# Kernel tuning notes

Measured on AMD Instinct MI355X. Metric: run time of the kernel, lower is better.

## Reference

```python
import jax, jax.numpy as jnp
import numpy as np

V, L, H, D, S, B = 32000, 6, 16, 1024, 512, 4
DK = D // H
DF = 4 * D
EPS = 1e-5


def setup_inputs() -> dict:
    key = jax.random.key(0)
    ks = jax.random.split(key, 24)
    std = 0.02
    def w(k, shape):
        return jax.random.normal(k, shape, dtype=jnp.float32) * std
    inp = {
        'x': jax.random.randint(ks[0], (B, S), 0, V),
        'tok_emb': w(ks[1], (V, D)),
        # per-layer params stacked on leading L axis; Linear stored as [in,out]
        'wq': w(ks[2], (L, D, D)), 'bq': jnp.zeros((L, D)),
        'wk': w(ks[3], (L, D, D)), 'bk': jnp.zeros((L, D)),
        'wv': w(ks[4], (L, D, D)), 'bv': jnp.zeros((L, D)),
        'wo': w(ks[5], (L, D, D)), 'bo': jnp.zeros((L, D)),
        'ln1_g': jnp.ones((L, D)), 'ln1_b': jnp.zeros((L, D)),
        'w1': w(ks[6], (L, D, DF)), 'b1': jnp.zeros((L, DF)),
        'w2': w(ks[7], (L, DF, D)), 'b2': jnp.zeros((L, D)),
        'ln2_g': jnp.ones((L, D)), 'ln2_b': jnp.zeros((L, D)),
        'lnf_g': jnp.ones((D,)), 'lnf_b': jnp.zeros((D,)),
        'lm_w': w(ks[8], (D, V)),
    }
    return inp


def _layernorm(x, g, b):
    mu = jnp.mean(x, axis=-1, keepdims=True)
    var = jnp.mean(jnp.square(x - mu), axis=-1, keepdims=True)
    return (x - mu) * jax.lax.rsqrt(var + EPS) * g + b


def _sinusoidal_pe(seq_len, d_model):
    pos = jnp.arange(seq_len, dtype=jnp.float32)[:, None]
    div = jnp.exp(jnp.arange(0, d_model, 2, dtype=jnp.float32) * (-np.log(10000.0) / d_model))
    pe = jnp.zeros((seq_len, d_model), dtype=jnp.float32)
    pe = pe.at[:, 0::2].set(jnp.sin(pos * div))
    pe = pe.at[:, 1::2].set(jnp.cos(pos * div))
    return pe  # [S, D]


def _gpt_forward(x, tok_emb, wq, bq, wk, bk, wv, bv, wo, bo,
                 ln1_g, ln1_b, w1, b1, w2, b2, ln2_g, ln2_b,
                 lnf_g, lnf_b, lm_w):
    b, s = x.shape
    h = tok_emb[x] + _sinusoidal_pe(s, D)  # [B,S,D]
    causal = jnp.tril(jnp.ones((s, s), dtype=bool))  # True = keep
    scale = 1.0 / np.sqrt(DK)

    def block(h, p):
        (wq, bq, wk, bk, wv, bv, wo, bo,
         ln1_g, ln1_b, w1, b1, w2, b2, ln2_g, ln2_b) = p
        hn = _layernorm(h, ln1_g, ln1_b)
        q = (hn @ wq + bq).reshape(b, s, H, DK)
        k = (hn @ wk + bk).reshape(b, s, H, DK)
        v = (hn @ wv + bv).reshape(b, s, H, DK)
        scores = jnp.einsum('bqhd,bkhd->bhqk', q, k) * scale
        scores = jnp.where(causal, scores, -1e9)
        attn = jax.nn.softmax(scores, axis=-1)
        ctx = jnp.einsum('bhqk,bkhd->bqhd', attn, v).reshape(b, s, D)
        h = h + (ctx @ wo + bo)
        hn2 = _layernorm(h, ln2_g, ln2_b)
        ff = jax.nn.gelu(hn2 @ w1 + b1, approximate=False) @ w2 + b2
        return h + ff, None

    params = (wq, bq, wk, bk, wv, bv, wo, bo,
              ln1_g, ln1_b, w1, b1, w2, b2, ln2_g, ln2_b)
    h, _ = jax.lax.scan(block, h, params)
    h = _layernorm(h, lnf_g, lnf_b)
    return h @ lm_w  # [B,S,V] logits


def reference(x, tok_emb, wq, bq, wk, bk, wv, bv, wo, bo,
              ln1_g, ln1_b, w1, b1, w2, b2, ln2_g, ln2_b,
              lnf_g, lnf_b, lm_w):
    return _gpt_forward(x, tok_emb, wq, bq, wk, bk, wv, bv, wo, bo,
                        ln1_g, ln1_b, w1, b1, w2, b2, ln2_g, ln2_b,
                        lnf_g, lnf_b, lm_w)
```

## Files before the change

kernel.cpp:

```cpp
#include <hip/hip_runtime.h>
#include <hip/hip_bf16.h>
#include <math.h>

#define V_SIZE 32000
#define L_NUM 6
#define H_NUM 16
#define D_MODEL 1024
#define S_LEN 512
#define B_SZ 4
#define DF_DIM 4096
#define ROWS (B_SZ * S_LEN)
#define QKV_N (3 * D_MODEL)
#define KVBLK 64
#define NJOB 12

typedef unsigned short u16;
typedef __attribute__((ext_vector_type(8))) short short8v;
typedef __attribute__((ext_vector_type(4))) float f32x4;

__device__ __forceinline__ float b2f(u16 b) {
  union { float f; unsigned u; } c; c.u = ((unsigned)b) << 16; return c.f;
}
__device__ __forceinline__ u16 f2b(float f) {
  __hip_bfloat16 h = __float2bfloat16(f);
  union { __hip_bfloat16 h; u16 u; } c; c.h = h; return c.u;
}
__device__ __forceinline__ void g2l16(const void* g, void* l) {
  __builtin_amdgcn_global_load_lds(
      (const __attribute__((address_space(1))) void*)g,
      (__attribute__((address_space(3))) void*)l, 16, 0, 0);
}

__global__ __launch_bounds__(256) void embed_kernel(
    const int* __restrict__ x, const float* __restrict__ tok_emb,
    float* __restrict__ h) {
  int row = blockIdx.x;
  int s = row % S_LEN;
  int tok = x[row];
  const float* te = tok_emb + (size_t)tok * D_MODEL;
  float* hr = h + (size_t)row * D_MODEL;
  float pos = (float)s;
  const float c = 9.210340371976184f / (float)D_MODEL;
#pragma unroll
  for (int i = 0; i < D_MODEL / 256; ++i) {
    int d = threadIdx.x + i * 256;
    float freq = expf(-(float)(d & ~1) * c);
    float ang = pos * freq;
    float pe = (d & 1) ? cosf(ang) : sinf(ang);
    hr[d] = te[d] + pe;
  }
}

__global__ __launch_bounds__(256) void layernorm_kernel(
    const float* __restrict__ in, const float* __restrict__ g,
    const float* __restrict__ b, u16* __restrict__ out) {
  const int row = blockIdx.x * 4 + (threadIdx.x >> 6);
  const int lane = threadIdx.x & 63;
  const float4* xr = (const float4*)(in + (size_t)row * D_MODEL);
  float4 v[4];
  float s1 = 0.f, s2 = 0.f;
#pragma unroll
  for (int i = 0; i < 4; ++i) {
    float4 t = xr[lane + i * 64];
    v[i] = t;
    s1 += t.x + t.y + t.z + t.w;
    s2 += t.x * t.x + t.y * t.y + t.z * t.z + t.w * t.w;
  }
#pragma unroll
  for (int off = 32; off; off >>= 1) {
    s1 += __shfl_xor(s1, off, 64);
    s2 += __shfl_xor(s2, off, 64);
  }
  const float mu = s1 * (1.0f / D_MODEL);
  const float var = s2 * (1.0f / D_MODEL) - mu * mu;
  const float rstd = rsqrtf(var + 1e-5f);
  u16* orow = out + (size_t)row * D_MODEL;
#pragma unroll
  for (int i = 0; i < 4; ++i) {
    const int d = (lane + i * 64) * 4;
    const float4 gv = *(const float4*)&g[d];
    const float4 bv = *(const float4*)&b[d];
    u16 o0 = f2b((v[i].x - mu) * rstd * gv.x + bv.x);
    u16 o1 = f2b((v[i].y - mu) * rstd * gv.y + bv.y);
    u16 o2 = f2b((v[i].z - mu) * rstd * gv.z + bv.z);
    u16 o3 = f2b((v[i].w - mu) * rstd * gv.w + bv.w);
    uint2 pk;
    pk.x = (unsigned)o0 | ((unsigned)o1 << 16);
    pk.y = (unsigned)o2 | ((unsigned)o3 << 16);
    *(uint2*)&orow[d] = pk;
  }
}

__global__ __launch_bounds__(256) void transpose_cvt(
    const float* __restrict__ W, u16* __restrict__ Wt, int K, int N,
    long out_stride) {
  __shared__ float t[64][33];
  const float* Wl = W + (size_t)blockIdx.z * K * N;
  u16* Wtl = Wt + (size_t)blockIdx.z * out_stride;
  const int n0 = blockIdx.x * 32, k0 = blockIdx.y * 64;
  const int tx = threadIdx.x & 31, ty = threadIdx.x >> 5;
#pragma unroll
  for (int i = 0; i < 64; i += 8)
    t[ty + i][tx] = Wl[(size_t)(k0 + ty + i) * N + n0 + tx];
  __syncthreads();
#pragma unroll
  for (int j = 0; j < 32; j += 8) {
    const int n = ty + j;
    u16 lo = f2b(t[2 * tx][n]);
    u16 hi = f2b(t[2 * tx + 1][n]);
    *(unsigned*)&Wtl[(size_t)(n0 + n) * K + k0 + 2 * tx] =
        (unsigned)lo | ((unsigned)hi << 16);
  }
}

__global__ __launch_bounds__(256) void pack_qkv_bias(
    const float* __restrict__ bq, const float* __restrict__ bk,
    const float* __restrict__ bv, float* __restrict__ out) {
  int i = blockIdx.x * 256 + threadIdx.x;
  int l = i / QKV_N, j = i % QKV_N;
  float v = (j < D_MODEL) ? bq[l * D_MODEL + j]
          : (j < 2 * D_MODEL) ? bk[l * D_MODEL + j - D_MODEL]
          : bv[l * D_MODEL + j - 2 * D_MODEL];
  out[i] = v;
}

template <int TM, int OUT_MODE, bool GELU_ACT, int SPLITK>
__global__ __launch_bounds__(256) void gemm_bf16(
    const u16* __restrict__ A, const u16* __restrict__ Bt,
    const float* __restrict__ bias, float* __restrict__ Cf,
    u16* __restrict__ Cb, int M, int N, int K) {
  constexpr int MF = TM / 32;
  constexpr int AINSTS = TM / 32;
  __shared__ __align__(16) u16 As[2][TM * 64];
  __shared__ __align__(16) u16 Bs[2][128 * 64];
  const int tid = threadIdx.x;
  const int wid = tid >> 6;
  const int lane = tid & 63;
  const int wr = wid >> 1, wc = wid & 1;
  const int nwg = gridDim.x;
  const int id = blockIdx.x;
  const int q = nwg >> 3, r = nwg & 7;
  const int xcd = id & 7, i0 = id >> 3;
  const int swz = (xcd < r ? xcd * (q + 1) : r * (q + 1) + (xcd - r) * q) + i0;
  const int kh = (SPLITK > 1) ? (swz & (SPLITK - 1)) : 0;
  const int rest = (SPLITK > 1) ? (swz >> 1) : swz;
  const int gm = M / TM;
  const int bm = rest % gm, bn = rest / gm;
  const int Ksub = K / SPLITK;
  const int rowi = lane >> 3;
  const int gsw = ((lane & 7) ^ rowi) * 8;
  const u16* Ag = A + (size_t)(bm * TM + wid * (TM / 4) + rowi) * K + kh * Ksub + gsw;
  const u16* Bg = Bt + (size_t)(bn * 128 + wid * 32 + rowi) * K + kh * Ksub + gsw;
  auto stage = [&](int buf, int k0) {
#pragma unroll
    for (int i = 0; i < AINSTS; ++i)
      g2l16(Ag + k0 + (size_t)(8 * i) * K, As[buf] + wid * (TM / 4) * 64 + i * 512);
#pragma unroll
    for (int i = 0; i < 4; ++i)
      g2l16(Bg + k0 + (size_t)(8 * i) * K, Bs[buf] + wid * 2048 + i * 512);
  };
  f32x4 acc[MF][4] = {};
  const int fr = lane & 15;
  const int hi = lane >> 4;
  stage(0, 0);
  __syncthreads();
  for (int k0 = 0; k0 < Ksub; k0 += 64) {
    const int cur = (k0 >> 6) & 1;
    if (k0 + 64 < Ksub) stage(cur ^ 1, k0 + 64);
    short8v a[MF][2], b[4][2];
#pragma unroll
    for (int m = 0; m < MF; ++m)
#pragma unroll
      for (int kk = 0; kk < 2; ++kk) {
        const int g = (kk * 4 + hi) ^ (fr & 7);
        a[m][kk] = *(const short8v*)&As[cur][(wr * (TM / 2) + m * 16 + fr) * 64 + g * 8];
      }
#pragma unroll
    for (int n = 0; n < 4; ++n)
#pragma unroll
      for (int kk = 0; kk < 2; ++kk) {
        const int g = (kk * 4 + hi) ^ (fr & 7);
        b[n][kk] = *(const short8v*)&Bs[cur][(wc * 64 + n * 16 + fr) * 64 + g * 8];
      }
    __builtin_amdgcn_s_setprio(1);
#pragma unroll
    for (int kk = 0; kk < 2; ++kk)
#pragma unroll
      for (int m = 0; m < MF; ++m)
#pragma unroll
        for (int n = 0; n < 4; ++n)
          acc[m][n] = __builtin_amdgcn_mfma_f32_16x16x32_bf16(a[m][kk], b[n][kk], acc[m][n], 0, 0, 0);
    __builtin_amdgcn_s_setprio(0);
    __syncthreads();
  }
  const int row0 = bm * TM + wr * (TM / 2) + hi * 4;
  const int col0 = bn * 128 + wc * 64 + fr;
#pragma unroll
  for (int m = 0; m < MF; ++m) {
#pragma unroll
    for (int n = 0; n < 4; ++n) {
      const int col = col0 + n * 16;
      float bv = (OUT_MODE == 2) ? 0.f : bias[col];
      if (SPLITK > 1 && kh != 0) bv = 0.f;
#pragma unroll
      for (int r2 = 0; r2 < 4; ++r2) {
        const int row = row0 + m * 16 + r2;
        float v = acc[m][n][r2] + bv;
        if (GELU_ACT) v = 0.5f * v * (1.0f + erff(v * 0.70710678118f));
        size_t idx = (size_t)row * N + col;
        if (OUT_MODE == 0) Cb[idx] = f2b(v);
        else if (OUT_MODE == 1) {
          if (SPLITK > 1) atomicAdd(&Cf[idx], v);
          else Cf[idx] += v;
        } else Cf[idx] = v;
      }
    }
  }
}

#define LDA_H(H)                                                            \
  _Pragma("unroll") for (int m = 0; m < 4; ++m)                             \
  _Pragma("unroll") for (int ks = 0; ks < 2; ++ks) {                        \
    const int row_ = wm * 128 + (H)*64 + m * 16 + fr;                       \
    const int g_ = (ks * 4 + hi) ^ (fr & 7);                                \
    a[m][ks] = *(const short8v*)&smem[cur * 16384 + row_ * 64 + g_ * 8];    \
  }
#define LDB_H(H)                                                            \
  _Pragma("unroll") for (int n = 0; n < 2; ++n)                             \
  _Pragma("unroll") for (int ks = 0; ks < 2; ++ks) {                        \
    const int row_ = wn * 64 + (H)*32 + n * 16 + fr;                        \
    const int g_ = (ks * 4 + hi) ^ (fr & 7);                                \
    b[n][ks] = *(const short8v*)&smem[32768 + cur * 16384 + row_ * 64 + g_ * 8]; \
  }
#define MFMA_CLUSTER(QA, QB)                                                \
  __builtin_amdgcn_s_barrier();                                             \
  asm volatile("s_waitcnt lgkmcnt(0)" ::: "memory");                        \
  __builtin_amdgcn_sched_barrier(0);                                        \
  __builtin_amdgcn_s_setprio(1);                                            \
  _Pragma("unroll") for (int ks = 0; ks < 2; ++ks)                          \
  _Pragma("unroll") for (int m = 0; m < 4; ++m)                             \
  _Pragma("unroll") for (int n = 0; n < 2; ++n)                             \
    acc[(QA)*4 + m][(QB)*2 + n] = __builtin_amdgcn_mfma_f32_16x16x32_bf16(  \
        a[m][ks], b[n][ks], acc[(QA)*4 + m][(QB)*2 + n], 0, 0, 0);          \
  __builtin_amdgcn_s_setprio(0);

__global__ __launch_bounds__(512, 2) void gemm256_lm(
    const u16* __restrict__ A, const u16* __restrict__ Bt,
    float* __restrict__ C, int M, int N, int K) {
  extern __shared__ __align__(16) u16 smem[];
  const int tid = threadIdx.x, wid = tid >> 6, lane = tid & 63;
  const int wm = wid >> 2, wn = wid & 3;
  const int fr = lane & 15, hi = lane >> 4;
  const int T = K / 64;
  const int nwg = gridDim.x, id = blockIdx.x;
  const int q = nwg >> 3, r = nwg & 7;
  const int xcd = id & 7, i0 = id >> 3;
  const int swz = (xcd < r ? xcd * (q + 1) : r * (q + 1) + (xcd - r) * q) + i0;
  const int gm = M / 256;
  const int bm = swz % gm, bn = swz / gm;
  const int rowA0 = bm * 256, rowB0 = bn * 256;
  const int rowoff = wid * 8 + (lane >> 3);
  const int gsw = ((lane & 7) ^ (lane >> 3)) * 8;
  auto stA = [&](int qq, int tt, int bb) {
    g2l16(A + (size_t)(rowA0 + qq * 64 + rowoff) * K + tt * 64 + gsw,
          smem + bb * 16384 + qq * 4096 + wid * 512);
  };
  auto stB = [&](int qq, int tt, int bb) {
    g2l16(Bt + (size_t)(rowB0 + qq * 64 + rowoff) * K + tt * 64 + gsw,
          smem + 32768 + bb * 16384 + qq * 4096 + wid * 512);
  };
  f32x4 acc[8][4] = {};
  stA(0, 0, 0); stA(2, 0, 0);
  stB(0, 0, 0); stB(1, 0, 0); stB(2, 0, 0); stB(3, 0, 0);
  stA(1, 0, 0); stA(3, 0, 0);
  if (T > 1) {
    stA(0, 1, 1); stA(2, 1, 1);
    asm volatile("s_waitcnt vmcnt(2)" ::: "memory");
  } else {
    asm volatile("s_waitcnt vmcnt(0)" ::: "memory");
  }
  __builtin_amdgcn_s_barrier();
  for (int t = 0; t < T; ++t) {
    const int cur = t & 1, nxt = cur ^ 1;
    short8v a[4][2], b[2][2];
    LDA_H(0); LDB_H(0);
    if (t + 1 < T) { stB(0, t + 1, nxt); stB(1, t + 1, nxt); }
    MFMA_CLUSTER(0, 0);
    __builtin_amdgcn_s_barrier();
    LDB_H(1);
    if (t + 1 < T) { stB(2, t + 1, nxt); stB(3, t + 1, nxt); }
    MFMA_CLUSTER(0, 1);
    __builtin_amdgcn_s_barrier();
    LDA_H(1);
    if (t + 1 < T) { stA(1, t + 1, nxt); stA(3, t + 1, nxt); }
    MFMA_CLUSTER(1, 1);
    __builtin_amdgcn_s_barrier();
    LDB_H(0);
    if (t + 2 < T) { stA(0, t + 2, cur); stA(2, t + 2, cur); }
    MFMA_CLUSTER(1, 0);
    if (t + 1 < T) {
      if (t + 2 < T) asm volatile("s_waitcnt vmcnt(2)" ::: "memory");
      else           asm volatile("s_waitcnt vmcnt(0)" ::: "memory");
      __builtin_amdgcn_s_barrier();
    }
  }
  float* lf = (float*)smem;
#pragma unroll
  for (int c = 0; c < 2; ++c) {
    __syncthreads();
    if (wm == c) {
#pragma unroll
      for (int m = 0; m < 8; ++m)
#pragma unroll
        for (int n = 0; n < 4; ++n)
#pragma unroll
          for (int rr = 0; rr < 4; ++rr)
            lf[(m * 16 + hi * 4 + rr) * 256 + wn * 64 + n * 16 + fr] =
                acc[m][n][rr];
    }
    __syncthreads();
#pragma unroll
    for (int i = 0; i < 16; ++i) {
      const int f = i * 2048 + tid * 4;
      const int rw = f >> 8, cl = f & 255;
      f32x4 v = *(const f32x4*)&lf[f];
      __builtin_nontemporal_store(
          v, (f32x4*)&C[(size_t)(rowA0 + c * 128 + rw) * N + rowB0 + cl]);
    }
  }
}

__global__ __launch_bounds__(256) void attn_part(
    const u16* __restrict__ qkv, float* __restrict__ Op,
    float* __restrict__ Ml) {
  __shared__ __align__(16) u16 smem[3 * 64 * 72];
  u16 (*Qs)[72] = (u16(*)[72])smem;
  u16 (*Ks)[72] = (u16(*)[72])(smem + 4608);
  u16 (*Vs)[72] = (u16(*)[72])(smem + 9216);
  const int job = blockIdx.x, bh = blockIdx.y;
  constexpr int qt_of[NJOB] = {0, 1, 2, 3, 4, 4, 5, 5, 6, 6, 7, 7};
  constexpr int ch_of[NJOB] = {0, 0, 0, 0, 0, 1, 0, 1, 0, 1, 0, 1};
  const int qt = qt_of[job], ch = ch_of[job];
  const int b = bh >> 4, h = bh & 15;
  const int tid = threadIdx.x, wid = tid >> 6, lane = tid & 63;
  const int fr = lane & 15, ko = (lane >> 4) * 8;
  u16 (*Ps)[72] = (u16(*)[72])(smem + wid * 1152);
  const size_t rb = (size_t)b * S_LEN;
  const int q0 = qt * 64;
  const int hq = h * 64;
  const int t_lo = ch * 4;
  const int t_hi = (qt + 1 < t_lo + 4) ? qt + 1 : t_lo + 4;
#pragma unroll
  for (int i = 0; i < 2; ++i) {
    int e = tid + i * 256, r = e >> 3, c = (e & 7) * 8;
    *(short8v*)&Qs[r][c] = *(const short8v*)&qkv[(rb + q0 + r) * QKV_N + hq + c];
  }
  __syncthreads();
  short8v qf[2];
#pragma unroll
  for (int ks = 0; ks < 2; ++ks)
    qf[ks] = *(const short8v*)&Qs[wid * 16 + fr][ks * 32 + ko];
  f32x4 acc_o[4] = {};
  float mrow[4], lrow[4];
#pragma unroll
  for (int r = 0; r < 4; ++r) { mrow[r] = -1e30f; lrow[r] = 0.f; }
  short8v kreg[2], vreg[2];
  auto loadregs = [&](int t) {
    const int k0 = t * KVBLK;
#pragma unroll
    for (int i = 0; i < 2; ++i) {
      const int e = tid + i * 256, rr = e >> 3, cc = (e & 7) * 8;
      kreg[i] = *(const short8v*)&qkv[(rb + k0 + rr) * QKV_N + D_MODEL + hq + cc];
      vreg[i] = *(const short8v*)&qkv[(rb + k0 + rr) * QKV_N + 2 * D_MODEL + hq + cc];
    }
  };
  loadregs(t_lo);
  for (int t = t_lo; t < t_hi; ++t) {
    __syncthreads();
#pragma unroll
    for (int i = 0; i < 2; ++i) {
      const int e = tid + i * 256, rr = e >> 3, cc = (e & 7) * 8;
      *(short8v*)&Ks[rr][cc] = kreg[i];
#pragma unroll
      for (int j = 0; j < 8; ++j) Vs[cc + j][rr] = (u16)vreg[i][j];
    }
    __syncthreads();
    if (t + 1 < t_hi) loadregs(t + 1);
    const int k0 = t * KVBLK;
    f32x4 s[4] = {};
    __builtin_amdgcn_s_setprio(1);
#pragma unroll
    for (int n = 0; n < 4; ++n)
#pragma unroll
      for (int ks = 0; ks < 2; ++ks) {
        short8v kf = *(const short8v*)&Ks[n * 16 + fr][ks * 32 + ko];
        s[n] = __builtin_amdgcn_mfma_f32_16x16x32_bf16(qf[ks], kf, s[n], 0, 0, 0);
      }
    __builtin_amdgcn_s_setprio(0);
    const int rbase = q0 + wid * 16 + (lane >> 4) * 4;
#pragma unroll
    for (int r = 0; r < 4; ++r) {
      const int row_g = rbase + r;
      float vmax = -1e30f;
#pragma unroll
      for (int n = 0; n < 4; ++n) {
        float v = s[n][r] * 0.125f;
        if (k0 + n * 16 + fr > row_g) v = -1e30f;
        s[n][r] = v;
        vmax = fmaxf(vmax, v);
      }
#pragma unroll
      for (int off = 1; off < 16; off <<= 1) vmax = fmaxf(vmax, __shfl_xor(vmax, off, 64));
      const float mnew = fmaxf(mrow[r], vmax);
      const float sc = expf(mrow[r] - mnew);
      mrow[r] = mnew;
      float ssum = 0.f;
#pragma unroll
      for (int n = 0; n < 4; ++n) {
        float p = expf(s[n][r] - mnew);
        s[n][r] = p;
        ssum += p;
      }
#pragma unroll
      for (int off = 1; off < 16; off <<= 1) ssum += __shfl_xor(ssum, off, 64);
      lrow[r] = lrow[r] * sc + ssum;
#pragma unroll
      for (int n = 0; n < 4; ++n) {
        acc_o[n][r] *= sc;
        Ps[(lane >> 4) * 4 + r][n * 16 + fr] = f2b(s[n][r]);
      }
    }
    __builtin_amdgcn_s_setprio(1);
#pragma unroll
    for (int ks = 0; ks < 2; ++ks) {
      short8v pf = *(const short8v*)&Ps[fr][ks * 32 + ko];
#pragma unroll
      for (int n = 0; n < 4; ++n) {
        short8v vf = *(const short8v*)&Vs[n * 16 + fr][ks * 32 + ko];
        acc_o[n] = __builtin_amdgcn_mfma_f32_16x16x32_bf16(pf, vf, acc_o[n], 0, 0, 0);
      }
    }
    __builtin_amdgcn_s_setprio(0);
  }
  const size_t jb = (size_t)(bh * NJOB + job);
#pragma unroll
  for (int r = 0; r < 4; ++r) {
    const int row_l = wid * 16 + (lane >> 4) * 4 + r;
    const size_t base = (jb * 64 + row_l) * 64;
#pragma unroll
    for (int n = 0; n < 4; ++n) Op[base + n * 16 + fr] = acc_o[n][r];
    if (fr == 0) {
      Ml[jb * 128 + row_l * 2] = mrow[r];
      Ml[jb * 128 + row_l * 2 + 1] = lrow[r];
    }
  }
}

__global__ __launch_bounds__(256) void attn_combine(
    const float* __restrict__ Op, const float* __restrict__ Ml,
    u16* __restrict__ ctx) {
  const int qt = blockIdx.x, bh = blockIdx.y;
  const int b = bh >> 4, h = bh & 15;
  constexpr int job0_of[8] = {0, 1, 2, 3, 4, 6, 8, 10};
  const int j0 = job0_of[qt];
  const bool two = qt >= 4;
  const size_t rb = (size_t)b * S_LEN;
  const int q0 = qt * 64, hq = h * 64;
  const size_t jb1 = (size_t)(bh * NJOB + j0);
  const size_t jb2 = jb1 + 1;
#pragma unroll
  for (int i = 0; i < 4; ++i) {
    const int idx4 = threadIdx.x + i * 256;
    const int row = idx4 >> 4, c4 = (idx4 & 15) * 4;
    f32x4 o1 = *(const f32x4*)&Op[(jb1 * 64 + row) * 64 + c4];
    const float m1 = Ml[jb1 * 128 + row * 2], l1 = Ml[jb1 * 128 + row * 2 + 1];
    float o[4];
    float inv;
    if (two) {
      f32x4 o2 = *(const f32x4*)&Op[(jb2 * 64 + row) * 64 + c4];
      const float m2 = Ml[jb2 * 128 + row * 2], l2 = Ml[jb2 * 128 + row * 2 + 1];
      const float m = fmaxf(m1, m2);
      const float e1 = expf(m1 - m), e2 = expf(m2 - m);
      inv = 1.0f / (l1 * e1 + l2 * e2);
#pragma unroll
      for (int j = 0; j < 4; ++j) o[j] = o1[j] * e1 + o2[j] * e2;
    } else {
      inv = 1.0f / l1;
#pragma unroll
      for (int j = 0; j < 4; ++j) o[j] = o1[j];
    }
    uint2 pk;
    pk.x = (unsigned)f2b(o[0] * inv) | ((unsigned)f2b(o[1] * inv) << 16);
    pk.y = (unsigned)f2b(o[2] * inv) | ((unsigned)f2b(o[3] * inv) << 16);
    *(uint2*)&ctx[(rb + q0 + row) * D_MODEL + hq + c4] = pk;
  }
}

extern "C" void kernel_launch(void* const* d_in, const int* in_sizes, int n_in,
                              void* d_out, int out_size, void* d_ws, size_t ws_size,
                              hipStream_t stream) {
  const int* x = (const int*)d_in[0];
  const float* tok_emb = (const float*)d_in[1];
  const float* wq = (const float*)d_in[2];
  const float* bq = (const float*)d_in[3];
  const float* wk = (const float*)d_in[4];
  const float* bk = (const float*)d_in[5];
  const float* wv = (const float*)d_in[6];
  const float* bv = (const float*)d_in[7];
  const float* wo = (const float*)d_in[8];
  const float* bo = (const float*)d_in[9];
  const float* ln1_g = (const float*)d_in[10];
  const float* ln1_b = (const float*)d_in[11];
  const float* w1 = (const float*)d_in[12];
  const float* b1 = (const float*)d_in[13];
  const float* w2 = (const float*)d_in[14];
  const float* b2 = (const float*)d_in[15];
  const float* ln2_g = (const float*)d_in[16];
  const float* ln2_b = (const float*)d_in[17];
  const float* lnf_g = (const float*)d_in[18];
  const float* lnf_b = (const float*)d_in[19];
  const float* lm_w = (const float*)d_in[20];

  char* w = (char*)d_ws;
  float* h    = (float*)(w);
  u16*  hn    = (u16*)(w + (8ll << 20));
  u16*  qkvb  = (u16*)(w + (12ll << 20));
  u16*  cbuf  = (u16*)(w + (24ll << 20));
  u16*  ff    = qkvb;
  u16*  wqkvT = (u16*)(w + (28ll << 20));
  u16*  woT   = (u16*)(w + (64ll << 20));
  u16*  w1T   = (u16*)(w + (76ll << 20));
  u16*  w2T   = (u16*)(w + (124ll << 20));
  u16*  lmT   = (u16*)(w + (172ll << 20));
  float* bqkv = (float*)(w + (235ll << 20));
  float* Op   = (float*)(w + (236ll << 20));
  float* Ml   = (float*)(w + (249ll << 20));

  const size_t DD = (size_t)D_MODEL * D_MODEL;
  const size_t DDF = (size_t)D_MODEL * DF_DIM;
  const long QS = (long)QKV_N * D_MODEL;
  transpose_cvt<<<dim3(32, 16, L_NUM), 256, 0, stream>>>(wq, wqkvT, D_MODEL, D_MODEL, QS);
  transpose_cvt<<<dim3(32, 16, L_NUM), 256, 0, stream>>>(wk, wqkvT + DD, D_MODEL, D_MODEL, QS);
  transpose_cvt<<<dim3(32, 16, L_NUM), 256, 0, stream>>>(wv, wqkvT + 2 * DD, D_MODEL, D_MODEL, QS);
  transpose_cvt<<<dim3(32, 16, L_NUM), 256, 0, stream>>>(wo, woT, D_MODEL, D_MODEL, (long)DD);
  transpose_cvt<<<dim3(128, 16, L_NUM), 256, 0, stream>>>(w1, w1T, D_MODEL, DF_DIM, (long)DDF);
  transpose_cvt<<<dim3(32, 64, L_NUM), 256, 0, stream>>>(w2, w2T, DF_DIM, D_MODEL, (long)DDF);
  transpose_cvt<<<dim3(V_SIZE / 32, 16, 1), 256, 0, stream>>>(lm_w, lmT, D_MODEL, V_SIZE, 0);
  pack_qkv_bias<<<L_NUM * QKV_N / 256, 256, 0, stream>>>(bq, bk, bv, bqkv);

  embed_kernel<<<ROWS, 256, 0, stream>>>(x, tok_emb, h);

  const int nQKV = (ROWS / 64) * (QKV_N / 128);
  const int nPRJ = 2 * (ROWS / 64) * (D_MODEL / 128);
  const int nFF1 = (ROWS / 64) * (DF_DIM / 128);
  const int nFF2 = 2 * (ROWS / 64) * (D_MODEL / 128);
  for (int l = 0; l < L_NUM; ++l) {
    layernorm_kernel<<<ROWS / 4, 256, 0, stream>>>(h, ln1_g + l * D_MODEL, ln1_b + l * D_MODEL, hn);
    gemm_bf16<64, 0, false, 1><<<nQKV, 256, 0, stream>>>(
        hn, wqkvT + (size_t)l * QS, bqkv + l * QKV_N, nullptr, qkvb,
        ROWS, QKV_N, D_MODEL);
    attn_part<<<dim3(NJOB, B_SZ * H_NUM), 256, 0, stream>>>(qkvb, Op, Ml);
    attn_combine<<<dim3(S_LEN / 64, B_SZ * H_NUM), 256, 0, stream>>>(Op, Ml, cbuf);
    gemm_bf16<64, 1, false, 2><<<nPRJ, 256, 0, stream>>>(
        cbuf, woT + l * DD, bo + l * D_MODEL, h, nullptr, ROWS, D_MODEL, D_MODEL);
    layernorm_kernel<<<ROWS / 4, 256, 0, stream>>>(h, ln2_g + l * D_MODEL, ln2_b + l * D_MODEL, hn);
    gemm_bf16<64, 0, true, 1><<<nFF1, 256, 0, stream>>>(
        hn, w1T + l * DDF, b1 + l * DF_DIM, nullptr, ff, ROWS, DF_DIM, D_MODEL);
    gemm_bf16<64, 1, false, 2><<<nFF2, 256, 0, stream>>>(
        ff, w2T + l * DDF, b2 + l * D_MODEL, h, nullptr, ROWS, D_MODEL, DF_DIM);
  }
  layernorm_kernel<<<ROWS / 4, 256, 0, stream>>>(h, lnf_g, lnf_b, hn);

  hipFuncSetAttribute((const void*)gemm256_lm,
                      hipFuncAttributeMaxDynamicSharedMemorySize, 131072);
  const int nLM = (ROWS / 256) * (V_SIZE / 256);
  gemm256_lm<<<nLM, 512, 131072, stream>>>(
      hn, lmT, (float*)d_out, ROWS, V_SIZE, D_MODEL);
}
```

Measured before the change: 1.373 ms.

## Merge weight transposes into one launch and write unsplit attention tiles directly

Replaces seven transpose_cvt launches with a single transpose_all kernel that maps a flat block index onto each weight's tile, cutting launch overhead and tail gaps. Attention query tiles that are not split (qt<4) now normalise and write bf16 context straight from attn_part, so attn_combine only handles the split tiles and fewer partial buffers go through global memory. It also switches expf to __expf in the softmax and drops the nontemporal hint on the LM-head stores. The fast exp trades a little accuracy, and the plain stores may change cache behaviour for the large logits output.

```diff
diff --git a/kernel.cpp b/kernel.cpp
--- a/kernel.cpp
+++ b/kernel.cpp
@@ -91,24 +91,58 @@
   }
 }
 
-__global__ __launch_bounds__(256) void transpose_cvt(
-    const float* __restrict__ W, u16* __restrict__ Wt, int K, int N,
-    long out_stride) {
+__global__ __launch_bounds__(256) void transpose_all(
+    const float* __restrict__ wq, const float* __restrict__ wk,
+    const float* __restrict__ wv, const float* __restrict__ wo,
+    const float* __restrict__ w1, const float* __restrict__ w2,
+    const float* __restrict__ lm_w,
+    u16* __restrict__ wqkvT, u16* __restrict__ woT,
+    u16* __restrict__ w1T, u16* __restrict__ w2T, u16* __restrict__ lmT) {
+  const size_t DD = (size_t)D_MODEL * D_MODEL;
+  const size_t DDF = (size_t)D_MODEL * DF_DIM;
+  const long QS = (long)QKV_N * D_MODEL;
+  int gid = blockIdx.x;
+  const float* src;
+  u16* dst;
+  int K, N, kt, nt;
+  if (gid < 12288) {
+    const int l = gid / 2048, rjob = gid % 2048;
+    const int which = rjob / 512, t = rjob % 512;
+    kt = t % 16; nt = t / 16;
+    K = D_MODEL; N = D_MODEL;
+    src = (which == 0 ? wq : which == 1 ? wk : which == 2 ? wv : wo) + l * DD;
+    dst = (which < 3) ? (wqkvT + l * QS + which * DD) : (woT + l * DD);
+  } else if (gid < 24576) {
+    const int idx = gid - 12288;
+    const int l = idx / 2048, t = idx % 2048;
+    kt = t % 16; nt = t / 16;
+    K = D_MODEL; N = DF_DIM;
+    src = w1 + l * DDF; dst = w1T + l * DDF;
+  } else if (gid < 36864) {
+    const int idx = gid - 24576;
+    const int l = idx / 2048, t = idx % 2048;
+    kt = t % 64; nt = t / 64;
+    K = DF_DIM; N = D_MODEL;
+    src = w2 + l * DDF; dst = w2T + l * DDF;
+  } else {
+    const int idx = gid - 36864;
+    kt = idx % 16; nt = idx / 16;
+    K = D_MODEL; N = V_SIZE;
+    src = lm_w; dst = lmT;
+  }
   __shared__ float t[64][33];
-  const float* Wl = W + (size_t)blockIdx.z * K * N;
-  u16* Wtl = Wt + (size_t)blockIdx.z * out_stride;
-  const int n0 = blockIdx.x * 32, k0 = blockIdx.y * 64;
+  const int n0 = nt * 32, k0 = kt * 64;
   const int tx = threadIdx.x & 31, ty = threadIdx.x >> 5;
 #pragma unroll
   for (int i = 0; i < 64; i += 8)
-    t[ty + i][tx] = Wl[(size_t)(k0 + ty + i) * N + n0 + tx];
+    t[ty + i][tx] = src[(size_t)(k0 + ty + i) * N + n0 + tx];
   __syncthreads();
 #pragma unroll
   for (int j = 0; j < 32; j += 8) {
     const int n = ty + j;
     u16 lo = f2b(t[2 * tx][n]);
     u16 hi = f2b(t[2 * tx + 1][n]);
-    *(unsigned*)&Wtl[(size_t)(n0 + n) * K + k0 + 2 * tx] =
+    *(unsigned*)&dst[(size_t)(n0 + n) * K + k0 + 2 * tx] =
         (unsigned)lo | ((unsigned)hi << 16);
   }
 }
@@ -324,15 +358,14 @@
       const int f = i * 2048 + tid * 4;
       const int rw = f >> 8, cl = f & 255;
       f32x4 v = *(const f32x4*)&lf[f];
-      __builtin_nontemporal_store(
-          v, (f32x4*)&C[(size_t)(rowA0 + c * 128 + rw) * N + rowB0 + cl]);
+      *(f32x4*)&C[(size_t)(rowA0 + c * 128 + rw) * N + rowB0 + cl] = v;
     }
   }
 }
 
 __global__ __launch_bounds__(256) void attn_part(
     const u16* __restrict__ qkv, float* __restrict__ Op,
-    float* __restrict__ Ml) {
+    float* __restrict__ Ml, u16* __restrict__ ctx) {
   __shared__ __align__(16) u16 smem[3 * 64 * 72];
   u16 (*Qs)[72] = (u16(*)[72])smem;
   u16 (*Ks)[72] = (u16(*)[72])(smem + 4608);
@@ -412,12 +445,12 @@
 #pragma unroll
       for (int off = 1; off < 16; off <<= 1) vmax = fmaxf(vmax, __shfl_xor(vmax, off, 64));
       const float mnew = fmaxf(mrow[r], vmax);
-      const float sc = expf(mrow[r] - mnew);
+      const float sc = __expf(mrow[r] - mnew);
       mrow[r] = mnew;
       float ssum = 0.f;
 #pragma unroll
       for (int n = 0; n < 4; ++n) {
-        float p = expf(s[n][r] - mnew);
+        float p = __expf(s[n][r] - mnew);
         s[n][r] = p;
         ssum += p;
       }
@@ -442,16 +475,27 @@
     }
     __builtin_amdgcn_s_setprio(0);
   }
-  const size_t jb = (size_t)(bh * NJOB + job);
-#pragma unroll
-  for (int r = 0; r < 4; ++r) {
-    const int row_l = wid * 16 + (lane >> 4) * 4 + r;
-    const size_t base = (jb * 64 + row_l) * 64;
-#pragma unroll
-    for (int n = 0; n < 4; ++n) Op[base + n * 16 + fr] = acc_o[n][r];
-    if (fr == 0) {
-      Ml[jb * 128 + row_l * 2] = mrow[r];
-      Ml[jb * 128 + row_l * 2 + 1] = lrow[r];
+  if (qt < 4) {
+#pragma unroll
+    for (int r = 0; r < 4; ++r) {
+      const int row_l = wid * 16 + (lane >> 4) * 4 + r;
+      const float inv = 1.0f / lrow[r];
+#pragma unroll
+      for (int n = 0; n < 4; ++n)
+        ctx[(rb + q0 + row_l) * D_MODEL + hq + n * 16 + fr] = f2b(acc_o[n][r] * inv);
+    }
+  } else {
+    const size_t jb = (size_t)(bh * NJOB + job);
+#pragma unroll
+    for (int r = 0; r < 4; ++r) {
+      const int row_l = wid * 16 + (lane >> 4) * 4 + r;
+      const size_t base = (jb * 64 + row_l) * 64;
+#pragma unroll
+      for (int n = 0; n < 4; ++n) Op[base + n * 16 + fr] = acc_o[n][r];
+      if (fr == 0) {
+        Ml[jb * 128 + row_l * 2] = mrow[r];
+        Ml[jb * 128 + row_l * 2 + 1] = lrow[r];
+      }
     }
   }
 }
@@ -459,11 +503,9 @@
 __global__ __launch_bounds__(256) void attn_combine(
     const float* __restrict__ Op, const float* __restrict__ Ml,
     u16* __restrict__ ctx) {
-  const int qt = blockIdx.x, bh = blockIdx.y;
+  const int qt = blockIdx.x + 4, bh = blockIdx.y;
   const int b = bh >> 4, h = bh & 15;
-  constexpr int job0_of[8] = {0, 1, 2, 3, 4, 6, 8, 10};
-  const int j0 = job0_of[qt];
-  const bool two = qt >= 4;
+  const int j0 = 4 + blockIdx.x * 2;
   const size_t rb = (size_t)b * S_LEN;
   const int q0 = qt * 64, hq = h * 64;
   const size_t jb1 = (size_t)(bh * NJOB + j0);
@@ -474,21 +516,14 @@
     const int row = idx4 >> 4, c4 = (idx4 & 15) * 4;
     f32x4 o1 = *(const f32x4*)&Op[(jb1 * 64 + row) * 64 + c4];
     const float m1 = Ml[jb1 * 128 + row * 2], l1 = Ml[jb1 * 128 + row * 2 + 1];
+    f32x4 o2 = *(const f32x4*)&Op[(jb2 * 64 + row) * 64 + c4];
+    const float m2 = Ml[jb2 * 128 + row * 2], l2 = Ml[jb2 * 128 + row * 2 + 1];
+    const float m = fmaxf(m1, m2);
+    const float e1 = __expf(m1 - m), e2 = __expf(m2 - m);
+    const float inv = 1.0f / (l1 * e1 + l2 * e2);
     float o[4];
-    float inv;
-    if (two) {
-      f32x4 o2 = *(const f32x4*)&Op[(jb2 * 64 + row) * 64 + c4];
-      const float m2 = Ml[jb2 * 128 + row * 2], l2 = Ml[jb2 * 128 + row * 2 + 1];
-      const float m = fmaxf(m1, m2);
-      const float e1 = expf(m1 - m), e2 = expf(m2 - m);
-      inv = 1.0f / (l1 * e1 + l2 * e2);
-#pragma unroll
-      for (int j = 0; j < 4; ++j) o[j] = o1[j] * e1 + o2[j] * e2;
-    } else {
-      inv = 1.0f / l1;
-#pragma unroll
-      for (int j = 0; j < 4; ++j) o[j] = o1[j];
-    }
+#pragma unroll
+    for (int j = 0; j < 4; ++j) o[j] = o1[j] * e1 + o2[j] * e2;
     uint2 pk;
     pk.x = (unsigned)f2b(o[0] * inv) | ((unsigned)f2b(o[1] * inv) << 16);
     pk.y = (unsigned)f2b(o[2] * inv) | ((unsigned)f2b(o[3] * inv) << 16);
@@ -536,20 +571,15 @@
   float* Op   = (float*)(w + (236ll << 20));
   float* Ml   = (float*)(w + (249ll << 20));
 
+  transpose_all<<<52864, 256, 0, stream>>>(
+      wq, wk, wv, wo, w1, w2, lm_w, wqkvT, woT, w1T, w2T, lmT);
+  pack_qkv_bias<<<L_NUM * QKV_N / 256, 256, 0, stream>>>(bq, bk, bv, bqkv);
+
+  embed_kernel<<<ROWS, 256, 0, stream>>>(x, tok_emb, h);
+
   const size_t DD = (size_t)D_MODEL * D_MODEL;
   const size_t DDF = (size_t)D_MODEL * DF_DIM;
   const long QS = (long)QKV_N * D_MODEL;
-  transpose_cvt<<<dim3(32, 16, L_NUM), 256, 0, stream>>>(wq, wqkvT, D_MODEL, D_MODEL, QS);
-  transpose_cvt<<<dim3(32, 16, L_NUM), 256, 0, stream>>>(wk, wqkvT + DD, D_MODEL, D_MODEL, QS);
-  transpose_cvt<<<dim3(32, 16, L_NUM), 256, 0, stream>>>(wv, wqkvT + 2 * DD, D_MODEL, D_MODEL, QS);
-  transpose_cvt<<<dim3(32, 16, L_NUM), 256, 0, stream>>>(wo, woT, D_MODEL, D_MODEL, (long)DD);
-  transpose_cvt<<<dim3(128, 16, L_NUM), 256, 0, stream>>>(w1, w1T, D_MODEL, DF_DIM, (long)DDF);
-  transpose_cvt<<<dim3(32, 64, L_NUM), 256, 0, stream>>>(w2, w2T, DF_DIM, D_MODEL, (long)DDF);
-  transpose_cvt<<<dim3(V_SIZE / 32, 16, 1), 256, 0, stream>>>(lm_w, lmT, D_MODEL, V_SIZE, 0);
-  pack_qkv_bias<<<L_NUM * QKV_N / 256, 256, 0, stream>>>(bq, bk, bv, bqkv);
-
-  embed_kernel<<<ROWS, 256, 0, stream>>>(x, tok_emb, h);
-
   const int nQKV = (ROWS / 64) * (QKV_N / 128);
   const int nPRJ = 2 * (ROWS / 64) * (D_MODEL / 128);
   const int nFF1 = (ROWS / 64) * (DF_DIM / 128);
@@ -559,8 +589,8 @@
     gemm_bf16<64, 0, false, 1><<<nQKV, 256, 0, stream>>>(
         hn, wqkvT + (size_t)l * QS, bqkv + l * QKV_N, nullptr, qkvb,
         ROWS, QKV_N, D_MODEL);
-    attn_part<<<dim3(NJOB, B_SZ * H_NUM), 256, 0, stream>>>(qkvb, Op, Ml);
-    attn_combine<<<dim3(S_LEN / 64, B_SZ * H_NUM), 256, 0, stream>>>(Op, Ml, cbuf);
+    attn_part<<<dim3(NJOB, B_SZ * H_NUM), 256, 0, stream>>>(qkvb, Op, Ml, cbuf);
+    attn_combine<<<dim3(4, B_SZ * H_NUM), 256, 0, stream>>>(Op, Ml, cbuf);
     gemm_bf16<64, 1, false, 2><<<nPRJ, 256, 0, stream>>>(
         cbuf, woT + l * DD, bo + l * D_MODEL, h, nullptr, ROWS, D_MODEL, D_MODEL);
     layernorm_kernel<<<ROWS / 4, 256, 0, stream>>>(h, ln2_g + l * D_MODEL, ln2_b + l * D_MODEL, hn);
```

New measurement: 1.350 ms (median of 2 runs). No clear change (-1.7%).
